# Optimization experiments

Hardware: AMD Instinct MI355X
Metric: run time of the kernel (lower is better)

The kernel has to match this reference:

```python
import jax, jax.numpy as jnp
import numpy as np

B, C, M = 1024, 64, 512  # batch, cluster_dim, num_clusters


def setup_inputs() -> dict:
    key = jax.random.key(0)
    k1, k2, k3 = jax.random.split(key, 3)
    x = jax.random.normal(k1, (B, C, M), dtype=jnp.float32)
    running_mean = jax.random.normal(k2, (1, C, M), dtype=jnp.float32) * 0.1
    # per-cluster whitening subspaces: identity + small symmetric perturbation
    A = jax.random.normal(k3, (M, C, C), dtype=jnp.float32) * 0.05
    subspaces = jnp.eye(C, dtype=jnp.float32)[None] + 0.5 * (A + jnp.swapaxes(A, -1, -2))
    return {"x": x, "running_mean": running_mean, "subspaces": subspaces}


def reference(x, running_mean, subspaces):
    # ZCANormSVDPI inference forward:
    #   x: (B, C, M); running_mean: (1, C, M); subspaces: (M, C, C)
    #   xc = x - running_mean; per-cluster m: z[m] = subspaces[m] @ xc[:, :, m]^T
    #   output permuted back to (B, C, M)
    xc = x - running_mean                      # (B, C, M)
    z = jnp.einsum('mcd,bdm->bcm', subspaces, xc)  # (B, C, M)
    return z
```

## Files before the change

kernel.cpp:

```cpp
#include <hip/hip_runtime.h>
#include <hip/hip_bf16.h>


typedef __attribute__((ext_vector_type(8))) short short8;
typedef __attribute__((ext_vector_type(4))) float f32x4;

namespace {
constexpr int Mm = 512, Cc = 64, Bb = 1024;
constexpr int MT = 16, BT = 16, NB = 8;
constexpr size_t LDSB = 65536 + 65536;

__device__ __forceinline__ short bfc(float f) {
  __hip_bfloat16 h = __float2bfloat16(f);
  union { __hip_bfloat16 b; short s; } u;
  u.b = h;
  return u.s;
}
__device__ __forceinline__ unsigned pack2(float a, float b) {
  return (unsigned)(unsigned short)bfc(a) |
         ((unsigned)(unsigned short)bfc(b) << 16);
}
__device__ __forceinline__ int xsw(int row, int c) {
  return c ^ (row & 7) ^ (((row >> 6) & 3) << 1);
}
}

#define ELEM(V, I) ((I) == 0 ? (V).x : (I) == 1 ? (V).y : (I) == 2 ? (V).z : (V).w)

__global__ __launch_bounds__(1024, 4) void zca_v12(
    const float* __restrict__ x, const float* __restrict__ mean,
    const float* __restrict__ S, float* __restrict__ out) {
  extern __shared__ unsigned char lds[];
  unsigned char* xb0 = lds;
  unsigned char* xb1 = lds + 32768;
  float* zl = (float*)(lds + 65536);

  const int tid = threadIdx.x;
  const int l = tid & 63;
  const int w = __builtin_amdgcn_readfirstlane(tid >> 6);

  const int id = blockIdx.x;
  const int sw = ((id & 7) << 5) + (id >> 3);
  const int m0 = (sw >> 3) * MT;
  const int b0 = (sw & 7) * (BT * NB);

  const int mq = tid & 3;
  const int u = (tid >> 2) & 15;
  const int bq = w >> 1;
  const int d2 = ((w & 1) << 5) + (u << 1);
  const int chunkS = ((w & 1) << 2) + (u >> 2);
  const int mqr = tid & 3;
  const int br = (tid >> 2) & 15;
  const int clow = (tid >> 6) & 15;

  float4 st0[4], st1[4];

#define ISSUE(ST, T)                                                          \
  {                                                                           \
    _Pragma("unroll") for (int dd = 0; dd < 2; ++dd)                          \
        _Pragma("unroll") for (int p = 0; p < 2; ++p)                         \
            ST[dd * 2 + p] = *(const float4*)(                                \
                x + (size_t)((b0 + (T)*BT + p * 8 + bq) * Cc + d2 + dd) * Mm  \
                  + m0 + mq * 4);                                             \
  }

#define STAGE(ST, XW)                                                         \
  {                                                                           \
    _Pragma("unroll") for (int p = 0; p < 2; ++p) {                           \
      _Pragma("unroll") for (int i = 0; i < 4; ++i) {                         \
        const int row = (mq * 4 + i) * BT + p * 8 + bq;                       \
        const unsigned v = pack2(ELEM(ST[p], i) - ELEM(mvE, i),               \
                                 ELEM(ST[2 + p], i) - ELEM(mvO, i));          \
        *(unsigned*)((XW) + row * 128 + xsw(row, chunkS) * 16 + (u & 3) * 4)  \
            = v;                                                              \
      }                                                                       \
    }                                                                         \
  }

#define BAR()                                          \
  {                                                    \
    asm volatile("s_waitcnt lgkmcnt(0)" ::: "memory"); \
    __builtin_amdgcn_s_barrier();                      \
  }

  ISSUE(st0, 0)
  ISSUE(st1, 1)
  const float4 mvE = *(const float4*)(mean + (size_t)d2 * Mm + m0 + mq * 4);
  const float4 mvO =
      *(const float4*)(mean + (size_t)(d2 + 1) * Mm + m0 + mq * 4);

  short8 A[4][2];
#pragma unroll
  for (int ct = 0; ct < 4; ++ct) {
#pragma unroll
    for (int ks = 0; ks < 2; ++ks) {
      const float* sp = S + ((size_t)(m0 + w) * Cc + ct * 16 + (l & 15)) * Cc +
                        ks * 32 + (l >> 4) * 8;
      const float4 f0 = *(const float4*)sp;
      const float4 f1 = *(const float4*)(sp + 4);
      short8 a;
      a[0] = bfc(f0.x); a[1] = bfc(f0.y); a[2] = bfc(f0.z); a[3] = bfc(f0.w);
      a[4] = bfc(f1.x); a[5] = bfc(f1.y); a[6] = bfc(f1.z); a[7] = bfc(f1.w);
      A[ct][ks] = a;
    }
  }
  STAGE(st0, xb0)
  BAR()

#define ZW()                                                                  \
  {                                                                           \
    const int h = l >> 4;                                                     \
    _Pragma("unroll") for (int ct = 0; ct < 4; ++ct) {                        \
      _Pragma("unroll") for (int r = 0; r < 4; ++r) {                         \
        const int vcol = (r ^ h ^ (w >> 2)) & 3;                              \
        zl[w * 1024 + ct * 256 + h * 64 + vcol * 16 + (l & 15)] =             \
            acc[ct][r];                                                       \
      }                                                                       \
    }                                                                         \
  }

#define ZR(T)                                                                 \
  {                                                                           \
    _Pragma("unroll") for (int t2 = 0; t2 < 4; ++t2) {                        \
      const int c_ = t2 * 16 + clow;                                          \
      const int h = (c_ >> 2) & 3, r = c_ & 3;                                \
      const int vcol = (r ^ h ^ mqr) & 3;                                     \
      float v[4];                                                             \
      _Pragma("unroll") for (int i = 0; i < 4; ++i)                           \
          v[i] = zl[(mqr * 4 + i) * 1024 + t2 * 256 + h * 64 + vcol * 16 +    \
                    br];                                                      \
      *(float4*)(out + (size_t)((b0 + (T)*BT + br) * Cc + c_) * Mm + m0 +     \
                 mqr * 4) = make_float4(v[0], v[1], v[2], v[3]);              \
    }                                                                         \
  }

#define ITER(T, XR, XW, STC, STN)                                              \
  {                                                                            \
    if ((T) + 2 < NB) ISSUE(STN, (T) + 2)                                      \
    const int rowB = w * BT + (l & 15);                                        \
    const short8 Bf0 = *(const short8*)(                                       \
        (XR) + rowB * 128 + xsw(rowB, (l >> 4)) * 16);                         \
    const short8 Bf1 = *(const short8*)(                                       \
        (XR) + rowB * 128 + xsw(rowB, 4 + (l >> 4)) * 16);                     \
    f32x4 acc[4];                                                              \
    _Pragma("unroll") for (int ct = 0; ct < 4; ++ct) acc[ct] =                 \
        (f32x4){0.f, 0.f, 0.f, 0.f};                                           \
    _Pragma("unroll") for (int ct = 0; ct < 4; ++ct) acc[ct] =                 \
        __builtin_amdgcn_mfma_f32_16x16x32_bf16(A[ct][0], Bf0, acc[ct], 0, 0,  \
                                                0);                            \
    _Pragma("unroll") for (int ct = 0; ct < 4; ++ct) acc[ct] =                 \
        __builtin_amdgcn_mfma_f32_16x16x32_bf16(A[ct][1], Bf1, acc[ct], 0, 0,  \
                                                0);                            \
    ZW()                                                                       \
    BAR()   \
    ZR(T)                                                                      \
    if ((T) + 1 < NB) STAGE(STC, XW)                                           \
    if ((T) + 1 < NB) BAR()    \
  }

  ITER(0, xb0, xb1, st1, st0)
  ITER(1, xb1, xb0, st0, st1)
  ITER(2, xb0, xb1, st1, st0)
  ITER(3, xb1, xb0, st0, st1)
  ITER(4, xb0, xb1, st1, st0)
  ITER(5, xb1, xb0, st0, st1)
  ITER(6, xb0, xb1, st1, st0)
  ITER(7, xb1, xb0, st0, st1)

#undef ITER
#undef ZR
#undef ZW
#undef BAR
#undef STAGE
#undef ISSUE
}

extern "C" void kernel_launch(void* const* d_in, const int* in_sizes, int n_in,
                              void* d_out, int out_size, void* d_ws,
                              size_t ws_size, hipStream_t stream) {
  const float* x = (const float*)d_in[0];
  const float* mean = (const float*)d_in[1];
  const float* S = (const float*)d_in[2];
  float* out = (float*)d_out;
  const int nblocks = (Mm / MT) * (Bb / (BT * NB));
  hipLaunchKernelGGL(zca_v12, dim3(nblocks), dim3(1024), LDSB, stream, x,
                     mean, S, out);
}
```

Before: 67.87 us.

## Double-buffer z staging and defer output store by one tile

```diff
diff --git a/kernel.cpp b/kernel.cpp
--- a/kernel.cpp
+++ b/kernel.cpp
@@ -8,7 +8,7 @@
 namespace {
 constexpr int Mm = 512, Cc = 64, Bb = 1024;
 constexpr int MT = 16, BT = 16, NB = 8;
-constexpr size_t LDSB = 65536 + 65536;
+constexpr size_t LDSB = 32768 + 2 * 65536;
 
 __device__ __forceinline__ short bfc(float f) {
   __hip_bfloat16 h = __float2bfloat16(f);
@@ -27,13 +27,13 @@
 
 #define ELEM(V, I) ((I) == 0 ? (V).x : (I) == 1 ? (V).y : (I) == 2 ? (V).z : (V).w)
 
-__global__ __launch_bounds__(1024, 4) void zca_v12(
+__global__ __launch_bounds__(1024, 4) void zca_v13(
     const float* __restrict__ x, const float* __restrict__ mean,
     const float* __restrict__ S, float* __restrict__ out) {
   extern __shared__ unsigned char lds[];
-  unsigned char* xb0 = lds;
-  unsigned char* xb1 = lds + 32768;
-  float* zl = (float*)(lds + 65536);
+  unsigned char* xl = lds;
+  float* zb0 = (float*)(lds + 32768);
+  float* zb1 = (float*)(lds + 98304);
 
   const int tid = threadIdx.x;
   const int l = tid & 63;
@@ -64,14 +64,14 @@
                   + m0 + mq * 4);                                             \
   }
 
-#define STAGE(ST, XW)                                                         \
+#define STAGE(ST)                                                             \
   {                                                                           \
     _Pragma("unroll") for (int p = 0; p < 2; ++p) {                           \
       _Pragma("unroll") for (int i = 0; i < 4; ++i) {                         \
         const int row = (mq * 4 + i) * BT + p * 8 + bq;                       \
         const unsigned v = pack2(ELEM(ST[p], i) - ELEM(mvE, i),               \
                                  ELEM(ST[2 + p], i) - ELEM(mvO, i));          \
-        *(unsigned*)((XW) + row * 128 + xsw(row, chunkS) * 16 + (u & 3) * 4)  \
+        *(unsigned*)(xl + row * 128 + xsw(row, chunkS) * 16 + (u & 3) * 4)    \
             = v;                                                              \
       }                                                                       \
     }                                                                         \
@@ -104,22 +104,22 @@
       A[ct][ks] = a;
     }
   }
-  STAGE(st0, xb0)
+  STAGE(st0)
   BAR()
 
-#define ZW()                                                                  \
+#define ZW(ZB)                                                                \
   {                                                                           \
     const int h = l >> 4;                                                     \
     _Pragma("unroll") for (int ct = 0; ct < 4; ++ct) {                        \
       _Pragma("unroll") for (int r = 0; r < 4; ++r) {                         \
         const int vcol = (r ^ h ^ (w >> 2)) & 3;                              \
-        zl[w * 1024 + ct * 256 + h * 64 + vcol * 16 + (l & 15)] =             \
+        (ZB)[w * 1024 + ct * 256 + h * 64 + vcol * 16 + (l & 15)] =           \
             acc[ct][r];                                                       \
       }                                                                       \
     }                                                                         \
   }
 
-#define ZR(T)                                                                 \
+#define ZR(ZB, TR)                                                            \
   {                                                                           \
     _Pragma("unroll") for (int t2 = 0; t2 < 4; ++t2) {                        \
       const int c_ = t2 * 16 + clow;                                          \
@@ -127,21 +127,21 @@
       const int vcol = (r ^ h ^ mqr) & 3;                                     \
       float v[4];                                                             \
       _Pragma("unroll") for (int i = 0; i < 4; ++i)                           \
-          v[i] = zl[(mqr * 4 + i) * 1024 + t2 * 256 + h * 64 + vcol * 16 +    \
-                    br];                                                      \
-      *(float4*)(out + (size_t)((b0 + (T)*BT + br) * Cc + c_) * Mm + m0 +     \
+          v[i] = (ZB)[(mqr * 4 + i) * 1024 + t2 * 256 + h * 64 + vcol * 16 +  \
+                      br];                                                    \
+      *(float4*)(out + (size_t)((b0 + (TR)*BT + br) * Cc + c_) * Mm + m0 +    \
                  mqr * 4) = make_float4(v[0], v[1], v[2], v[3]);              \
     }                                                                         \
   }
 
-#define ITER(T, XR, XW, STC, STN)                                              \
+#define ITER(T, ZBW, ZBR, STC, STN)                                            \
   {                                                                            \
     if ((T) + 2 < NB) ISSUE(STN, (T) + 2)                                      \
     const int rowB = w * BT + (l & 15);                                        \
     const short8 Bf0 = *(const short8*)(                                       \
-        (XR) + rowB * 128 + xsw(rowB, (l >> 4)) * 16);                         \
+        xl + rowB * 128 + xsw(rowB, (l >> 4)) * 16);                           \
     const short8 Bf1 = *(const short8*)(                                       \
-        (XR) + rowB * 128 + xsw(rowB, 4 + (l >> 4)) * 16);                     \
+        xl + rowB * 128 + xsw(rowB, 4 + (l >> 4)) * 16);                       \
     f32x4 acc[4];                                                              \
     _Pragma("unroll") for (int ct = 0; ct < 4; ++ct) acc[ct] =                 \
         (f32x4){0.f, 0.f, 0.f, 0.f};                                           \
@@ -151,21 +151,25 @@
     _Pragma("unroll") for (int ct = 0; ct < 4; ++ct) acc[ct] =                 \
         __builtin_amdgcn_mfma_f32_16x16x32_bf16(A[ct][1], Bf1, acc[ct], 0, 0,  \
                                                 0);                            \
-    ZW()                                                                       \
-    BAR()   \
-    ZR(T)                                                                      \
-    if ((T) + 1 < NB) STAGE(STC, XW)                                           \
-    if ((T) + 1 < NB) BAR()    \
+    ZW(ZBW)                                                                    \
+    if ((T) > 0) ZR(ZBR, (T)-1)                                                \
+    BAR()                                                                      \
+    if ((T) + 1 < NB) {                                                        \
+      STAGE(STC)                                                               \
+      BAR()                                                                    \
+    }                                                                          \
   }
 
-  ITER(0, xb0, xb1, st1, st0)
-  ITER(1, xb1, xb0, st0, st1)
-  ITER(2, xb0, xb1, st1, st0)
-  ITER(3, xb1, xb0, st0, st1)
-  ITER(4, xb0, xb1, st1, st0)
-  ITER(5, xb1, xb0, st0, st1)
-  ITER(6, xb0, xb1, st1, st0)
-  ITER(7, xb1, xb0, st0, st1)
+  ITER(0, zb0, zb1, st1, st0)
+  ITER(1, zb1, zb0, st0, st1)
+  ITER(2, zb0, zb1, st1, st0)
+  ITER(3, zb1, zb0, st0, st1)
+  ITER(4, zb0, zb1, st1, st0)
+  ITER(5, zb1, zb0, st0, st1)
+  ITER(6, zb0, zb1, st1, st0)
+  ITER(7, zb1, zb0, st0, st1)
+
+  ZR(zb1, 7)
 
 #undef ITER
 #undef ZR
@@ -183,6 +187,6 @@
   const float* S = (const float*)d_in[2];
   float* out = (float*)d_out;
   const int nblocks = (Mm / MT) * (Bb / (BT * NB));
-  hipLaunchKernelGGL(zca_v12, dim3(nblocks), dim3(1024), LDSB, stream, x,
+  hipLaunchKernelGGL(zca_v13, dim3(nblocks), dim3(1024), LDSB, stream, x,
                      mean, S, out);
 }
```

Measured after the change: 71.66 us. +5.6%, slower.

## Split z staging into two LDS halves and overlap readout across iterations

Applied to the files above, without the earlier changes.

```diff
diff --git a/kernel.cpp b/kernel.cpp
--- a/kernel.cpp
+++ b/kernel.cpp
@@ -27,13 +27,14 @@
 
 #define ELEM(V, I) ((I) == 0 ? (V).x : (I) == 1 ? (V).y : (I) == 2 ? (V).z : (V).w)
 
-__global__ __launch_bounds__(1024, 4) void zca_v12(
+__global__ __launch_bounds__(1024, 4) void zca_v15(
     const float* __restrict__ x, const float* __restrict__ mean,
     const float* __restrict__ S, float* __restrict__ out) {
   extern __shared__ unsigned char lds[];
   unsigned char* xb0 = lds;
   unsigned char* xb1 = lds + 32768;
-  float* zl = (float*)(lds + 65536);
+  float* zA = (float*)(lds + 65536);
+  float* zB = (float*)(lds + 98304);
 
   const int tid = threadIdx.x;
   const int l = tid & 63;
@@ -107,29 +108,29 @@
   STAGE(st0, xb0)
   BAR()
 
-#define ZW()                                                                  \
+#define ZWH(ZBUF, H)                                                          \
   {                                                                           \
     const int h = l >> 4;                                                     \
-    _Pragma("unroll") for (int ct = 0; ct < 4; ++ct) {                        \
+    _Pragma("unroll") for (int ct2 = 0; ct2 < 2; ++ct2) {                     \
       _Pragma("unroll") for (int r = 0; r < 4; ++r) {                         \
         const int vcol = (r ^ h ^ (w >> 2)) & 3;                              \
-        zl[w * 1024 + ct * 256 + h * 64 + vcol * 16 + (l & 15)] =             \
-            acc[ct][r];                                                       \
+        (ZBUF)[w * 512 + ct2 * 256 + h * 64 + vcol * 16 + (l & 15)] =         \
+            acc[(H)*2 + ct2][r];                                              \
       }                                                                       \
     }                                                                         \
   }
 
-#define ZR(T)                                                                 \
+#define ZRH(ZBUF, H, TR)                                                      \
   {                                                                           \
-    _Pragma("unroll") for (int t2 = 0; t2 < 4; ++t2) {                        \
-      const int c_ = t2 * 16 + clow;                                          \
+    _Pragma("unroll") for (int t2 = 0; t2 < 2; ++t2) {                        \
+      const int c_ = ((H)*2 + t2) * 16 + clow;                                \
       const int h = (c_ >> 2) & 3, r = c_ & 3;                                \
       const int vcol = (r ^ h ^ mqr) & 3;                                     \
       float v[4];                                                             \
       _Pragma("unroll") for (int i = 0; i < 4; ++i)                           \
-          v[i] = zl[(mqr * 4 + i) * 1024 + t2 * 256 + h * 64 + vcol * 16 +    \
-                    br];                                                      \
-      *(float4*)(out + (size_t)((b0 + (T)*BT + br) * Cc + c_) * Mm + m0 +     \
+          v[i] = (ZBUF)[(mqr * 4 + i) * 512 + t2 * 256 + h * 64 + vcol * 16 + \
+                        br];                                                  \
+      *(float4*)(out + (size_t)((b0 + (TR)*BT + br) * Cc + c_) * Mm + m0 +    \
                  mqr * 4) = make_float4(v[0], v[1], v[2], v[3]);              \
     }                                                                         \
   }
@@ -151,11 +152,13 @@
     _Pragma("unroll") for (int ct = 0; ct < 4; ++ct) acc[ct] =                 \
         __builtin_amdgcn_mfma_f32_16x16x32_bf16(A[ct][1], Bf1, acc[ct], 0, 0,  \
                                                 0);                            \
-    ZW()                                                                       \
-    BAR()   \
-    ZR(T)                                                                      \
+    ZWH(zA, 0)                                                                 \
+    if ((T) > 0) ZRH(zB, 1, (T)-1)                                             \
+    BAR()                                                                      \
+    ZWH(zB, 1)                                                                 \
+    ZRH(zA, 0, T)                                                              \
     if ((T) + 1 < NB) STAGE(STC, XW)                                           \
-    if ((T) + 1 < NB) BAR()    \
+    BAR()                                                                      \
   }
 
   ITER(0, xb0, xb1, st1, st0)
@@ -167,9 +170,11 @@
   ITER(6, xb0, xb1, st1, st0)
   ITER(7, xb1, xb0, st0, st1)
 
+  ZRH(zB, 1, 7)
+
 #undef ITER
-#undef ZR
-#undef ZW
+#undef ZRH
+#undef ZWH
 #undef BAR
 #undef STAGE
 #undef ISSUE
@@ -183,6 +188,6 @@
   const float* S = (const float*)d_in[2];
   float* out = (float*)d_out;
   const int nblocks = (Mm / MT) * (Bb / (BT * NB));
-  hipLaunchKernelGGL(zca_v12, dim3(nblocks), dim3(1024), LDSB, stream, x,
+  hipLaunchKernelGGL(zca_v15, dim3(nblocks), dim3(1024), LDSB, stream, x,
                      mean, S, out);
 }
```

Measured after the change: 71.66 us. +5.6%, slower.
